# Optimization experiments

Measured on AMD Instinct MI355X. Metric: run time of the kernel, lower is better.

The kernel has to match this reference:

```python
import jax, jax.numpy as jnp
import numpy as np

B, N, D = 2, 2048, 768
H = 12
DH = D // H
SCALE = DH ** -0.5


def setup_inputs() -> dict:
    key = jax.random.key(0)
    k1, k2, k3 = jax.random.split(key, 3)
    x = jax.random.normal(k1, (B, N, D), dtype=jnp.float32)
    w_qkv = jax.random.normal(k2, (D, 3 * D), dtype=jnp.float32) * (D ** -0.5)
    b_qkv = jnp.zeros((3 * D,), dtype=jnp.float32)
    w_proj = jax.random.normal(k3, (D, D), dtype=jnp.float32) * (D ** -0.5)
    b_proj = jnp.zeros((D,), dtype=jnp.float32)
    return {"x": x, "w_qkv": w_qkv, "b_qkv": b_qkv, "w_proj": w_proj, "b_proj": b_proj}


def reference(x, w_qkv, b_qkv, w_proj, b_proj):
    b, n, d = x.shape
    # qkv: (B, n, 3, H, DH) -> (3, B, H, n, DH)
    qkv = (x @ w_qkv + b_qkv).reshape(b, n, 3, H, DH).transpose(2, 0, 3, 1, 4)
    q, k, v = qkv[0], qkv[1], qkv[2]
    # naive full attention matrix (B, H, n, n)
    attn = jnp.einsum('bhqd,bhkd->bhqk', q, k) * SCALE
    attn = jax.nn.softmax(attn, axis=-1)
    out = jnp.einsum('bhqk,bhkd->bhqd', attn, v)  # (B, H, n, DH)
    out = out.transpose(0, 2, 1, 3).reshape(b, n, d)
    return out @ w_proj + b_proj
```

## Files before the change

kernel.cpp:

```cpp
#include <hip/hip_runtime.h>


#define CB 2
#define CN 2048
#define CD 768
#define CH 12
#define CDH 64
#define CEXPSCALE 0.18033688f

typedef __bf16 bf16x8 __attribute__((ext_vector_type(8)));
typedef float f32x4 __attribute__((ext_vector_type(4)));
typedef unsigned short u16x8 __attribute__((ext_vector_type(8)));

static __device__ __forceinline__ unsigned short f2bf(float f) {
  union { float f; unsigned u; } v; v.f = f;
  unsigned r = v.u + 0x7fffu + ((v.u >> 16) & 1u);
  return (unsigned short)(r >> 16);
}

static __device__ __forceinline__ void gld_lds16(const unsigned short* g, unsigned short* lds_base) {
  __builtin_amdgcn_global_load_lds(
      (const __attribute__((address_space(1))) unsigned int*)g,
      (__attribute__((address_space(3))) unsigned int*)(unsigned int)(unsigned long long)lds_base,
      16, 0, 0);
}

__global__ __launch_bounds__(256) void cvt8(const float* __restrict__ src,
                                            unsigned short* __restrict__ dst) {
  size_t i = ((size_t)blockIdx.x * 256 + threadIdx.x) * 8;
  f32x4 a = *(const f32x4*)&src[i];
  f32x4 b = *(const f32x4*)&src[i + 4];
  u16x8 o;
#pragma unroll
  for (int j = 0; j < 4; ++j) { o[j] = f2bf(a[j]); o[4 + j] = f2bf(b[j]); }
  *(u16x8*)&dst[i] = o;
}

__global__ __launch_bounds__(256) void transpose_cvt(const float* __restrict__ src,
                                                     unsigned short* __restrict__ dst,
                                                     int R, int C) {
  __shared__ __align__(16) unsigned short t[64][72];
  const int c0 = blockIdx.x * 64, r0 = blockIdx.y * 64;
  const int tid = threadIdx.x;
#pragma unroll
  for (int i = 0; i < 4; ++i) {
    int c = tid + i * 256;
    int row = c >> 4, cc = (c & 15) * 4;
    f32x4 v = *(const f32x4*)&src[(size_t)(r0 + row) * C + c0 + cc];
#pragma unroll
    for (int j = 0; j < 4; ++j) t[row][cc + j] = f2bf(v[j]);
  }
  __syncthreads();
#pragma unroll
  for (int i = 0; i < 2; ++i) {
    int c = tid + i * 256;
    int drow = c >> 3, rc = (c & 7) * 8;
    u16x8 v;
#pragma unroll
    for (int j = 0; j < 8; ++j) v[j] = t[rc + j][drow];
    *(u16x8*)&dst[(size_t)(c0 + drow) * R + r0 + rc] = v;
  }
}

__global__ __launch_bounds__(256) void gemm128(const unsigned short* __restrict__ A,
                                               const unsigned short* __restrict__ Bt,
                                               const float* __restrict__ bias,
                                               int M, int N, int K, int mode,
                                               unsigned short* __restrict__ o0,
                                               unsigned short* __restrict__ o1,
                                               unsigned short* __restrict__ o2,
                                               float* __restrict__ outF) {
  __shared__ __align__(16) unsigned short As[128 * 32];
  __shared__ __align__(16) unsigned short Bs[128 * 32];
  const int tid = threadIdx.x;
  const int w = tid >> 6, lane = tid & 63, quad = lane >> 4, lc = lane & 15;
  const int wm = (w >> 1) * 64, wn = (w & 1) * 64;
  const int row0 = blockIdx.y * 128, col0 = blockIdx.x * 128;
  f32x4 acc[4][4] = {};

  const int rl = lane >> 2, cl = lane & 3;
  const int gc = cl ^ ((rl >> 1) & 3);
  const int rsw = (lc >> 1) & 3;

  for (int k0 = 0; k0 < K; k0 += 32) {
#pragma unroll
    for (int j = 0; j < 2; ++j) {
      int r = w * 32 + j * 16 + rl;
      gld_lds16(&A[(size_t)(row0 + r) * K + k0 + gc * 8], &As[(w * 32 + j * 16) * 32]);
      gld_lds16(&Bt[(size_t)(col0 + r) * K + k0 + gc * 8], &Bs[(w * 32 + j * 16) * 32]);
    }
    __syncthreads();
    bf16x8 af[4], bfv[4];
#pragma unroll
    for (int mt = 0; mt < 4; ++mt)
      af[mt] = *(const bf16x8*)&As[(wm + mt * 16 + lc) * 32 + (quad ^ rsw) * 8];
#pragma unroll
    for (int nt = 0; nt < 4; ++nt)
      bfv[nt] = *(const bf16x8*)&Bs[(wn + nt * 16 + lc) * 32 + (quad ^ rsw) * 8];
#pragma unroll
    for (int mt = 0; mt < 4; ++mt)
#pragma unroll
      for (int nt = 0; nt < 4; ++nt)
        acc[mt][nt] = __builtin_amdgcn_mfma_f32_16x16x32_bf16(af[mt], bfv[nt], acc[mt][nt], 0, 0, 0);
    __syncthreads();
  }

#pragma unroll
  for (int mt = 0; mt < 4; ++mt) {
#pragma unroll
    for (int nt = 0; nt < 4; ++nt) {
#pragma unroll
      for (int r = 0; r < 4; ++r) {
        int i = row0 + wm + mt * 16 + quad * 4 + r;
        int j = col0 + wn + nt * 16 + lc;
        float v = acc[mt][nt][r] + bias[j];
        if (mode == 0) {
          int b = i >> 11, n = i & 2047;
          int sec = j / 768;
          int within = j - sec * 768;
          int h = within >> 6, d = within & 63;
          int bh = b * CH + h;
          if (sec == 0)      o0[((size_t)bh * CN + n) * CDH + d] = f2bf(v);
          else if (sec == 1) o1[((size_t)bh * CN + n) * CDH + d] = f2bf(v);
          else               o2[((size_t)bh * CDH + d) * CN + n] = f2bf(v);
        } else {
          outF[(size_t)i * N + j] = v;
        }
      }
    }
  }
}

__global__ __launch_bounds__(256, 3) void attn64(const unsigned short* __restrict__ Q,
                                                 const unsigned short* __restrict__ K,
                                                 const unsigned short* __restrict__ Vt,
                                                 unsigned short* __restrict__ O) {
  __shared__ __align__(16) unsigned short Kls[2][64 * 64];
  __shared__ __align__(16) unsigned short Vls[2][64 * 64];
  __shared__ __align__(16) unsigned short P[4][16][88];
  const int bh = blockIdx.x, qt = blockIdx.y;
  const int tid = threadIdx.x;
  const int w = tid >> 6, lane = tid & 63, quad = lane >> 4, lc = lane & 15;
  const unsigned short* Qb = Q + (size_t)bh * CN * CDH;
  const unsigned short* Kb = K + (size_t)bh * CN * CDH;
  const unsigned short* Vb = Vt + (size_t)bh * CDH * CN;
  const int q0 = qt * 64 + w * 16;

  const int sr = lane >> 3, sc = lane & 7;
  const int sg = sc ^ sr;
  const int ksw = lc & 7;
  const int c0r = quad ^ ksw;
  const int c1r = c0r ^ 4;

  bf16x8 qf0 = *(const bf16x8*)&Qb[(size_t)(q0 + lc) * CDH + quad * 8];
  bf16x8 qf1 = *(const bf16x8*)&Qb[(size_t)(q0 + lc) * CDH + 32 + quad * 8];

  f32x4 o[4] = {};
  float rs = 0.f;

#pragma unroll
  for (int j2 = 0; j2 < 2; ++j2) {
    int j = w * 2 + j2;
    int r = j * 8 + sr;
    gld_lds16(&Kb[(size_t)r * CDH + sg * 8], &Kls[0][j * 8 * 64]);
    gld_lds16(&Vb[(size_t)r * CN + 0 + sg * 8], &Vls[0][j * 8 * 64]);
  }

  for (int kt = 0; kt < CN / 64; ++kt) {
    const int bb = kt & 1;
    __syncthreads();
    if (kt + 1 < CN / 64) {
      const int kn = (kt + 1) * 64;
#pragma unroll
      for (int j2 = 0; j2 < 2; ++j2) {
        int j = w * 2 + j2;
        int r = j * 8 + sr;
        gld_lds16(&Kb[(size_t)(kn + r) * CDH + sg * 8], &Kls[bb ^ 1][j * 8 * 64]);
        gld_lds16(&Vb[(size_t)r * CN + kn + sg * 8], &Vls[bb ^ 1][j * 8 * 64]);
      }
    }
#pragma unroll
    for (int t = 0; t < 4; ++t) {
      bf16x8 kf0 = *(const bf16x8*)&Kls[bb][(t * 16 + lc) * 64 + c0r * 8];
      bf16x8 kf1 = *(const bf16x8*)&Kls[bb][(t * 16 + lc) * 64 + c1r * 8];
      f32x4 z = {0.f, 0.f, 0.f, 0.f};
      z = __builtin_amdgcn_mfma_f32_16x16x32_bf16(kf0, qf0, z, 0, 0, 0);
      z = __builtin_amdgcn_mfma_f32_16x16x32_bf16(kf1, qf1, z, 0, 0, 0);
      float p0 = exp2f(z[0] * CEXPSCALE);
      float p1 = exp2f(z[1] * CEXPSCALE);
      float p2 = exp2f(z[2] * CEXPSCALE);
      float p3 = exp2f(z[3] * CEXPSCALE);
      rs += (p0 + p1) + (p2 + p3);
      unsigned d0 = __builtin_amdgcn_perm(__float_as_uint(p1), __float_as_uint(p0), 0x07060302u);
      unsigned d1 = __builtin_amdgcn_perm(__float_as_uint(p3), __float_as_uint(p2), 0x07060302u);
      uint2 dd; dd.x = d0; dd.y = d1;
      *(uint2*)&P[w][lc][t * 16 + quad * 4] = dd;
    }
    asm volatile("s_waitcnt lgkmcnt(0)" ::: "memory");
    bf16x8 pf0 = *(const bf16x8*)&P[w][lc][quad * 8];
    bf16x8 pf1 = *(const bf16x8*)&P[w][lc][32 + quad * 8];
#pragma unroll
    for (int dt = 0; dt < 4; ++dt) {
      bf16x8 vf0 = *(const bf16x8*)&Vls[bb][(dt * 16 + lc) * 64 + c0r * 8];
      bf16x8 vf1 = *(const bf16x8*)&Vls[bb][(dt * 16 + lc) * 64 + c1r * 8];
      o[dt] = __builtin_amdgcn_mfma_f32_16x16x32_bf16(pf0, vf0, o[dt], 0, 0, 0);
      o[dt] = __builtin_amdgcn_mfma_f32_16x16x32_bf16(pf1, vf1, o[dt], 0, 0, 0);
    }
  }

  rs += __shfl_xor(rs, 16, 64);
  rs += __shfl_xor(rs, 32, 64);
  const int b = bh / CH, h = bh - b * CH;
#pragma unroll
  for (int r = 0; r < 4; ++r) {
    float lr = __shfl(rs, quad * 4 + r, 64);
    float inv = 1.0f / lr;
#pragma unroll
    for (int dt = 0; dt < 4; ++dt) {
      int i = b * CN + q0 + quad * 4 + r;
      int j = h * CDH + dt * 16 + lc;
      O[(size_t)i * CD + j] = f2bf(o[dt][r] * inv);
    }
  }
}

extern "C" void kernel_launch(void* const* d_in, const int* in_sizes, int n_in,
                              void* d_out, int out_size, void* d_ws, size_t ws_size,
                              hipStream_t stream) {
  const float* x      = (const float*)d_in[0];
  const float* w_qkv  = (const float*)d_in[1];
  const float* b_qkv  = (const float*)d_in[2];
  const float* w_proj = (const float*)d_in[3];
  const float* b_proj = (const float*)d_in[4];
  float* out = (float*)d_out;
  unsigned short* ws = (unsigned short*)d_ws;

  unsigned short* xb      = ws;
  unsigned short* wqkv_t  = xb + (size_t)4096 * 768;
  unsigned short* wproj_t = wqkv_t + (size_t)2304 * 768;
  unsigned short* Qs  = wproj_t + (size_t)768 * 768;
  unsigned short* Ks  = Qs  + (size_t)CB * CH * CN * CDH;
  unsigned short* Vts = Ks  + (size_t)CB * CH * CN * CDH;
  unsigned short* AO  = Vts + (size_t)CB * CH * CN * CDH;

  cvt8<<<(4096 * 768) / (256 * 8), 256, 0, stream>>>(x, xb);
  transpose_cvt<<<dim3(2304 / 64, 768 / 64), 256, 0, stream>>>(w_qkv, wqkv_t, 768, 2304);
  transpose_cvt<<<dim3(768 / 64, 768 / 64), 256, 0, stream>>>(w_proj, wproj_t, 768, 768);
  gemm128<<<dim3(2304 / 128, 4096 / 128), 256, 0, stream>>>(
      xb, wqkv_t, b_qkv, 4096, 2304, 768, 0, Qs, Ks, Vts, nullptr);
  attn64<<<dim3(CB * CH, CN / 64), 256, 0, stream>>>(Qs, Ks, Vts, AO);
  gemm128<<<dim3(768 / 128, 4096 / 128), 256, 0, stream>>>(
      AO, wproj_t, b_proj, 4096, 768, 768, 1, nullptr, nullptr, nullptr, out);
}
```

Measured before the change: 192.5 us.

## Process two query subtiles per wave in attention and stage V-transpose stores through LDS

Each attention wave now handles 32 query rows as two 16-row subtiles, so every K/V fragment read from LDS feeds twice as many MFMAs and the grid is halved. The softmax scale is folded into Q inside the QKV GEMM epilogue, which removes a multiply per score. The transposed V output of the QKV GEMM is staged through dynamic shared memory so global stores are 16-byte contiguous instead of scattered 2-byte writes. The trade-off is higher register pressure in attention, fewer blocks to spread across CUs, and an extra barrier plus LDS round trip in the GEMM epilogue.

```diff
diff --git a/kernel.cpp b/kernel.cpp
--- a/kernel.cpp
+++ b/kernel.cpp
@@ -62,6 +62,7 @@
   }
 }
 
+extern __shared__ __align__(16) unsigned short smem[];
 __global__ __launch_bounds__(256) void gemm128(const unsigned short* __restrict__ A,
                                                const unsigned short* __restrict__ Bt,
                                                const float* __restrict__ bias,
@@ -70,8 +71,9 @@
                                                unsigned short* __restrict__ o1,
                                                unsigned short* __restrict__ o2,
                                                float* __restrict__ outF) {
-  __shared__ __align__(16) unsigned short As[128 * 32];
-  __shared__ __align__(16) unsigned short Bs[128 * 32];
+  unsigned short* As = smem;
+  unsigned short* Bs = smem + 128 * 32;
+  unsigned short* Ct = smem;
   const int tid = threadIdx.x;
   const int w = tid >> 6, lane = tid & 63, quad = lane >> 4, lc = lane & 15;
   const int wm = (w >> 1) * 64, wn = (w & 1) * 64;
@@ -105,26 +107,57 @@
     __syncthreads();
   }
 
-#pragma unroll
-  for (int mt = 0; mt < 4; ++mt) {
-#pragma unroll
-    for (int nt = 0; nt < 4; ++nt) {
-#pragma unroll
-      for (int r = 0; r < 4; ++r) {
-        int i = row0 + wm + mt * 16 + quad * 4 + r;
-        int j = col0 + wn + nt * 16 + lc;
-        float v = acc[mt][nt][r] + bias[j];
-        if (mode == 0) {
-          int b = i >> 11, n = i & 2047;
-          int sec = j / 768;
-          int within = j - sec * 768;
-          int h = within >> 6, d = within & 63;
-          int bh = b * CH + h;
-          if (sec == 0)      o0[((size_t)bh * CN + n) * CDH + d] = f2bf(v);
-          else if (sec == 1) o1[((size_t)bh * CN + n) * CDH + d] = f2bf(v);
-          else               o2[((size_t)bh * CDH + d) * CN + n] = f2bf(v);
-        } else {
-          outF[(size_t)i * N + j] = v;
+  if (mode == 0 && col0 >= 1536) {
+#pragma unroll
+    for (int mt = 0; mt < 4; ++mt) {
+#pragma unroll
+      for (int nt = 0; nt < 4; ++nt) {
+        int jl = wn + nt * 16 + lc;
+        int il0 = wm + mt * 16 + quad * 4;
+        unsigned short a0 = f2bf(acc[mt][nt][0] + bias[col0 + jl]);
+        unsigned short a1 = f2bf(acc[mt][nt][1] + bias[col0 + jl]);
+        unsigned short a2 = f2bf(acc[mt][nt][2] + bias[col0 + jl]);
+        unsigned short a3 = f2bf(acc[mt][nt][3] + bias[col0 + jl]);
+        uint2 dd;
+        dd.x = (unsigned)a0 | ((unsigned)a1 << 16);
+        dd.y = (unsigned)a2 | ((unsigned)a3 << 16);
+        *(uint2*)&Ct[jl * 136 + il0] = dd;
+      }
+    }
+    __syncthreads();
+    const int b = row0 >> 11, n0 = row0 & 2047;
+#pragma unroll
+    for (int i = 0; i < 8; ++i) {
+      int c = tid + i * 256;
+      int jl = c >> 4, cc = (c & 15) * 8;
+      u16x8 v = *(const u16x8*)&Ct[jl * 136 + cc];
+      int jcol = col0 - 1536 + jl;
+      int h = jcol >> 6, d = jcol & 63;
+      size_t gr = ((size_t)(b * CH + h) * CDH + d);
+      *(u16x8*)&o2[gr * CN + n0 + cc] = v;
+    }
+  } else {
+#pragma unroll
+    for (int mt = 0; mt < 4; ++mt) {
+#pragma unroll
+      for (int nt = 0; nt < 4; ++nt) {
+#pragma unroll
+        for (int r = 0; r < 4; ++r) {
+          int i = row0 + wm + mt * 16 + quad * 4 + r;
+          int j = col0 + wn + nt * 16 + lc;
+          float v = acc[mt][nt][r] + bias[j];
+          if (mode == 0) {
+            int b = i >> 11, n = i & 2047;
+            int sec = j >> 9 >= 3 ? (j >= 1536 ? 2 : 1) : (j >= 768 ? 1 : 0);
+            sec = (j >= 1536) ? 2 : (j >= 768 ? 1 : 0);
+            int within = j - sec * 768;
+            int h = within >> 6, d = within & 63;
+            int bh = b * CH + h;
+            if (sec == 0)      o0[((size_t)bh * CN + n) * CDH + d] = f2bf(v * CEXPSCALE);
+            else               o1[((size_t)bh * CN + n) * CDH + d] = f2bf(v);
+          } else {
+            outF[(size_t)i * N + j] = v;
+          }
         }
       }
     }
@@ -137,14 +170,14 @@
                                                  unsigned short* __restrict__ O) {
   __shared__ __align__(16) unsigned short Kls[2][64 * 64];
   __shared__ __align__(16) unsigned short Vls[2][64 * 64];
-  __shared__ __align__(16) unsigned short P[4][16][88];
+  __shared__ __align__(16) unsigned short P[4][2][16 * 72];
   const int bh = blockIdx.x, qt = blockIdx.y;
   const int tid = threadIdx.x;
   const int w = tid >> 6, lane = tid & 63, quad = lane >> 4, lc = lane & 15;
   const unsigned short* Qb = Q + (size_t)bh * CN * CDH;
   const unsigned short* Kb = K + (size_t)bh * CN * CDH;
   const unsigned short* Vb = Vt + (size_t)bh * CDH * CN;
-  const int q0 = qt * 64 + w * 16;
+  const int q0 = qt * 128 + w * 32;
 
   const int sr = lane >> 3, sc = lane & 7;
   const int sg = sc ^ sr;
@@ -152,11 +185,15 @@
   const int c0r = quad ^ ksw;
   const int c1r = c0r ^ 4;
 
-  bf16x8 qf0 = *(const bf16x8*)&Qb[(size_t)(q0 + lc) * CDH + quad * 8];
-  bf16x8 qf1 = *(const bf16x8*)&Qb[(size_t)(q0 + lc) * CDH + 32 + quad * 8];
-
-  f32x4 o[4] = {};
-  float rs = 0.f;
+  bf16x8 qf[2][2];
+#pragma unroll
+  for (int s = 0; s < 2; ++s) {
+    qf[s][0] = *(const bf16x8*)&Qb[(size_t)(q0 + s * 16 + lc) * CDH + quad * 8];
+    qf[s][1] = *(const bf16x8*)&Qb[(size_t)(q0 + s * 16 + lc) * CDH + 32 + quad * 8];
+  }
+
+  f32x4 o[2][4] = {};
+  float rs[2] = {0.f, 0.f};
 
 #pragma unroll
   for (int j2 = 0; j2 < 2; ++j2) {
@@ -183,43 +220,57 @@
     for (int t = 0; t < 4; ++t) {
       bf16x8 kf0 = *(const bf16x8*)&Kls[bb][(t * 16 + lc) * 64 + c0r * 8];
       bf16x8 kf1 = *(const bf16x8*)&Kls[bb][(t * 16 + lc) * 64 + c1r * 8];
-      f32x4 z = {0.f, 0.f, 0.f, 0.f};
-      z = __builtin_amdgcn_mfma_f32_16x16x32_bf16(kf0, qf0, z, 0, 0, 0);
-      z = __builtin_amdgcn_mfma_f32_16x16x32_bf16(kf1, qf1, z, 0, 0, 0);
-      float p0 = exp2f(z[0] * CEXPSCALE);
-      float p1 = exp2f(z[1] * CEXPSCALE);
-      float p2 = exp2f(z[2] * CEXPSCALE);
-      float p3 = exp2f(z[3] * CEXPSCALE);
-      rs += (p0 + p1) + (p2 + p3);
-      unsigned d0 = __builtin_amdgcn_perm(__float_as_uint(p1), __float_as_uint(p0), 0x07060302u);
-      unsigned d1 = __builtin_amdgcn_perm(__float_as_uint(p3), __float_as_uint(p2), 0x07060302u);
-      uint2 dd; dd.x = d0; dd.y = d1;
-      *(uint2*)&P[w][lc][t * 16 + quad * 4] = dd;
+#pragma unroll
+      for (int s = 0; s < 2; ++s) {
+        f32x4 z = {0.f, 0.f, 0.f, 0.f};
+        z = __builtin_amdgcn_mfma_f32_16x16x32_bf16(kf0, qf[s][0], z, 0, 0, 0);
+        z = __builtin_amdgcn_mfma_f32_16x16x32_bf16(kf1, qf[s][1], z, 0, 0, 0);
+        float p0 = exp2f(z[0]);
+        float p1 = exp2f(z[1]);
+        float p2 = exp2f(z[2]);
+        float p3 = exp2f(z[3]);
+        rs[s] += (p0 + p1) + (p2 + p3);
+        unsigned d0 = __builtin_amdgcn_perm(__float_as_uint(p1), __float_as_uint(p0), 0x07060302u);
+        unsigned d1 = __builtin_amdgcn_perm(__float_as_uint(p3), __float_as_uint(p2), 0x07060302u);
+        uint2 dd; dd.x = d0; dd.y = d1;
+        *(uint2*)&P[w][s][lc * 72 + t * 16 + quad * 4] = dd;
+      }
     }
     asm volatile("s_waitcnt lgkmcnt(0)" ::: "memory");
-    bf16x8 pf0 = *(const bf16x8*)&P[w][lc][quad * 8];
-    bf16x8 pf1 = *(const bf16x8*)&P[w][lc][32 + quad * 8];
+    bf16x8 pf[2][2];
+#pragma unroll
+    for (int s = 0; s < 2; ++s) {
+      pf[s][0] = *(const bf16x8*)&P[w][s][lc * 72 + quad * 8];
+      pf[s][1] = *(const bf16x8*)&P[w][s][lc * 72 + 32 + quad * 8];
+    }
 #pragma unroll
     for (int dt = 0; dt < 4; ++dt) {
       bf16x8 vf0 = *(const bf16x8*)&Vls[bb][(dt * 16 + lc) * 64 + c0r * 8];
       bf16x8 vf1 = *(const bf16x8*)&Vls[bb][(dt * 16 + lc) * 64 + c1r * 8];
-      o[dt] = __builtin_amdgcn_mfma_f32_16x16x32_bf16(pf0, vf0, o[dt], 0, 0, 0);
-      o[dt] = __builtin_amdgcn_mfma_f32_16x16x32_bf16(pf1, vf1, o[dt], 0, 0, 0);
-    }
-  }
-
-  rs += __shfl_xor(rs, 16, 64);
-  rs += __shfl_xor(rs, 32, 64);
+#pragma unroll
+      for (int s = 0; s < 2; ++s) {
+        o[s][dt] = __builtin_amdgcn_mfma_f32_16x16x32_bf16(pf[s][0], vf0, o[s][dt], 0, 0, 0);
+        o[s][dt] = __builtin_amdgcn_mfma_f32_16x16x32_bf16(pf[s][1], vf1, o[s][dt], 0, 0, 0);
+      }
+    }
+  }
+
   const int b = bh / CH, h = bh - b * CH;
 #pragma unroll
-  for (int r = 0; r < 4; ++r) {
-    float lr = __shfl(rs, quad * 4 + r, 64);
-    float inv = 1.0f / lr;
-#pragma unroll
-    for (int dt = 0; dt < 4; ++dt) {
-      int i = b * CN + q0 + quad * 4 + r;
-      int j = h * CDH + dt * 16 + lc;
-      O[(size_t)i * CD + j] = f2bf(o[dt][r] * inv);
+  for (int s = 0; s < 2; ++s) {
+    float r2 = rs[s];
+    r2 += __shfl_xor(r2, 16, 64);
+    r2 += __shfl_xor(r2, 32, 64);
+#pragma unroll
+    for (int r = 0; r < 4; ++r) {
+      float lr = __shfl(r2, quad * 4 + r, 64);
+      float inv = 1.0f / lr;
+#pragma unroll
+      for (int dt = 0; dt < 4; ++dt) {
+        int i = b * CN + q0 + s * 16 + quad * 4 + r;
+        int j = h * CDH + dt * 16 + lc;
+        O[(size_t)i * CD + j] = f2bf(o[s][dt][r] * inv);
+      }
     }
   }
 }
@@ -243,12 +294,15 @@
   unsigned short* Vts = Ks  + (size_t)CB * CH * CN * CDH;
   unsigned short* AO  = Vts + (size_t)CB * CH * CN * CDH;
 
+  const size_t smem_qkv  = (size_t)(128 * 136) * 2;
+  const size_t smem_proj = (size_t)(128 * 32 * 2) * 2;
+
   cvt8<<<(4096 * 768) / (256 * 8), 256, 0, stream>>>(x, xb);
   transpose_cvt<<<dim3(2304 / 64, 768 / 64), 256, 0, stream>>>(w_qkv, wqkv_t, 768, 2304);
   transpose_cvt<<<dim3(768 / 64, 768 / 64), 256, 0, stream>>>(w_proj, wproj_t, 768, 768);
-  gemm128<<<dim3(2304 / 128, 4096 / 128), 256, 0, stream>>>(
+  gemm128<<<dim3(2304 / 128, 4096 / 128), 256, smem_qkv, stream>>>(
       xb, wqkv_t, b_qkv, 4096, 2304, 768, 0, Qs, Ks, Vts, nullptr);
-  attn64<<<dim3(CB * CH, CN / 64), 256, 0, stream>>>(Qs, Ks, Vts, AO);
-  gemm128<<<dim3(768 / 128, 4096 / 128), 256, 0, stream>>>(
+  attn64<<<dim3(CB * CH, CN / 128), 256, 0, stream>>>(Qs, Ks, Vts, AO);
+  gemm128<<<dim3(768 / 128, 4096 / 128), 256, smem_proj, stream>>>(
       AO, wproj_t, b_proj, 4096, 768, 768, 1, nullptr, nullptr, nullptr, out);
 }
```

New measurement: 207.0 us. 1.08x slower.

## Fuse prep kernels, stage V-transpose epilogue through LDS, fold softmax scale into Q

Applied to the files above, without the earlier changes.

The three conversion kernels (x cast, w_qkv and w_proj transpose-casts) are merged into one prep launch to save launch overhead. In the QKV GEMM, the V section's transposed output is first staged in LDS and then written with coalesced 16-byte stores, replacing scattered 2-byte strided writes. The softmax exp scale is folded into Q at the GEMM epilogue, which removes a multiply per score in the attention inner loop. The cost is a larger dynamic shared-memory allocation for the QKV GEMM, which may reduce occupancy, and a slight change in Q rounding.

```diff
diff --git a/kernel.cpp b/kernel.cpp
--- a/kernel.cpp
+++ b/kernel.cpp
@@ -25,23 +25,28 @@
       16, 0, 0);
 }
 
-__global__ __launch_bounds__(256) void cvt8(const float* __restrict__ src,
-                                            unsigned short* __restrict__ dst) {
-  size_t i = ((size_t)blockIdx.x * 256 + threadIdx.x) * 8;
-  f32x4 a = *(const f32x4*)&src[i];
-  f32x4 b = *(const f32x4*)&src[i + 4];
-  u16x8 o;
-#pragma unroll
-  for (int j = 0; j < 4; ++j) { o[j] = f2bf(a[j]); o[4 + j] = f2bf(b[j]); }
-  *(u16x8*)&dst[i] = o;
-}
-
-__global__ __launch_bounds__(256) void transpose_cvt(const float* __restrict__ src,
-                                                     unsigned short* __restrict__ dst,
-                                                     int R, int C) {
+__global__ __launch_bounds__(256) void prep(const float* __restrict__ x,
+                                            unsigned short* __restrict__ xb,
+                                            const float* __restrict__ w_qkv,
+                                            unsigned short* __restrict__ wqkv_t,
+                                            const float* __restrict__ w_proj,
+                                            unsigned short* __restrict__ wproj_t) {
   __shared__ __align__(16) unsigned short t[64][72];
-  const int c0 = blockIdx.x * 64, r0 = blockIdx.y * 64;
-  const int tid = threadIdx.x;
+  const int bid = blockIdx.x, tid = threadIdx.x;
+#pragma unroll
+  for (int it = 0; it < 2; ++it) {
+    size_t i = ((size_t)(bid * 2 + it) * 256 + tid) * 8;
+    f32x4 a = *(const f32x4*)&x[i];
+    f32x4 b = *(const f32x4*)&x[i + 4];
+    u16x8 o;
+#pragma unroll
+    for (int j = 0; j < 4; ++j) { o[j] = f2bf(a[j]); o[4 + j] = f2bf(b[j]); }
+    *(u16x8*)&xb[i] = o;
+  }
+  if (bid >= 576) return;
+  const float* src; unsigned short* dst; int R, C, c0, r0;
+  if (bid < 432) { src = w_qkv; dst = wqkv_t; R = 768; C = 2304; c0 = (bid % 36) * 64; r0 = (bid / 36) * 64; }
+  else { int u = bid - 432; src = w_proj; dst = wproj_t; R = 768; C = 768; c0 = (u % 12) * 64; r0 = (u / 12) * 64; }
 #pragma unroll
   for (int i = 0; i < 4; ++i) {
     int c = tid + i * 256;
@@ -62,6 +67,7 @@
   }
 }
 
+extern __shared__ __align__(16) unsigned short smem[];
 __global__ __launch_bounds__(256) void gemm128(const unsigned short* __restrict__ A,
                                                const unsigned short* __restrict__ Bt,
                                                const float* __restrict__ bias,
@@ -70,8 +76,9 @@
                                                unsigned short* __restrict__ o1,
                                                unsigned short* __restrict__ o2,
                                                float* __restrict__ outF) {
-  __shared__ __align__(16) unsigned short As[128 * 32];
-  __shared__ __align__(16) unsigned short Bs[128 * 32];
+  unsigned short* As = smem;
+  unsigned short* Bs = smem + 128 * 32;
+  unsigned short* Ct = smem;
   const int tid = threadIdx.x;
   const int w = tid >> 6, lane = tid & 63, quad = lane >> 4, lc = lane & 15;
   const int wm = (w >> 1) * 64, wn = (w & 1) * 64;
@@ -105,26 +112,57 @@
     __syncthreads();
   }
 
-#pragma unroll
-  for (int mt = 0; mt < 4; ++mt) {
-#pragma unroll
-    for (int nt = 0; nt < 4; ++nt) {
-#pragma unroll
-      for (int r = 0; r < 4; ++r) {
-        int i = row0 + wm + mt * 16 + quad * 4 + r;
-        int j = col0 + wn + nt * 16 + lc;
-        float v = acc[mt][nt][r] + bias[j];
-        if (mode == 0) {
-          int b = i >> 11, n = i & 2047;
-          int sec = j / 768;
-          int within = j - sec * 768;
-          int h = within >> 6, d = within & 63;
-          int bh = b * CH + h;
-          if (sec == 0)      o0[((size_t)bh * CN + n) * CDH + d] = f2bf(v);
-          else if (sec == 1) o1[((size_t)bh * CN + n) * CDH + d] = f2bf(v);
-          else               o2[((size_t)bh * CDH + d) * CN + n] = f2bf(v);
-        } else {
-          outF[(size_t)i * N + j] = v;
+  if (mode == 0 && col0 >= 1536) {
+#pragma unroll
+    for (int mt = 0; mt < 4; ++mt) {
+#pragma unroll
+      for (int nt = 0; nt < 4; ++nt) {
+        int jl = wn + nt * 16 + lc;
+        int il0 = wm + mt * 16 + quad * 4;
+        float bj = bias[col0 + jl];
+        unsigned short a0 = f2bf(acc[mt][nt][0] + bj);
+        unsigned short a1 = f2bf(acc[mt][nt][1] + bj);
+        unsigned short a2 = f2bf(acc[mt][nt][2] + bj);
+        unsigned short a3 = f2bf(acc[mt][nt][3] + bj);
+        uint2 dd;
+        dd.x = (unsigned)a0 | ((unsigned)a1 << 16);
+        dd.y = (unsigned)a2 | ((unsigned)a3 << 16);
+        *(uint2*)&Ct[jl * 136 + il0] = dd;
+      }
+    }
+    __syncthreads();
+    const int b = row0 >> 11, n0 = row0 & 2047;
+#pragma unroll
+    for (int i = 0; i < 8; ++i) {
+      int c = tid + i * 256;
+      int jl = c >> 4, cc = (c & 15) * 8;
+      u16x8 v = *(const u16x8*)&Ct[jl * 136 + cc];
+      int jcol = col0 - 1536 + jl;
+      int h = jcol >> 6, d = jcol & 63;
+      size_t gr = ((size_t)(b * CH + h) * CDH + d);
+      *(u16x8*)&o2[gr * CN + n0 + cc] = v;
+    }
+  } else {
+#pragma unroll
+    for (int mt = 0; mt < 4; ++mt) {
+#pragma unroll
+      for (int nt = 0; nt < 4; ++nt) {
+#pragma unroll
+        for (int r = 0; r < 4; ++r) {
+          int i = row0 + wm + mt * 16 + quad * 4 + r;
+          int j = col0 + wn + nt * 16 + lc;
+          float v = acc[mt][nt][r] + bias[j];
+          if (mode == 0) {
+            int b = i >> 11, n = i & 2047;
+            int sec = (j >= 768) ? 1 : 0;
+            int within = j - sec * 768;
+            int h = within >> 6, d = within & 63;
+            int bh = b * CH + h;
+            if (sec == 0) o0[((size_t)bh * CN + n) * CDH + d] = f2bf(v * CEXPSCALE);
+            else          o1[((size_t)bh * CN + n) * CDH + d] = f2bf(v);
+          } else {
+            outF[(size_t)i * N + j] = v;
+          }
         }
       }
     }
@@ -186,10 +224,10 @@
       f32x4 z = {0.f, 0.f, 0.f, 0.f};
       z = __builtin_amdgcn_mfma_f32_16x16x32_bf16(kf0, qf0, z, 0, 0, 0);
       z = __builtin_amdgcn_mfma_f32_16x16x32_bf16(kf1, qf1, z, 0, 0, 0);
-      float p0 = exp2f(z[0] * CEXPSCALE);
-      float p1 = exp2f(z[1] * CEXPSCALE);
-      float p2 = exp2f(z[2] * CEXPSCALE);
-      float p3 = exp2f(z[3] * CEXPSCALE);
+      float p0 = exp2f(z[0]);
+      float p1 = exp2f(z[1]);
+      float p2 = exp2f(z[2]);
+      float p3 = exp2f(z[3]);
       rs += (p0 + p1) + (p2 + p3);
       unsigned d0 = __builtin_amdgcn_perm(__float_as_uint(p1), __float_as_uint(p0), 0x07060302u);
       unsigned d1 = __builtin_amdgcn_perm(__float_as_uint(p3), __float_as_uint(p2), 0x07060302u);
@@ -243,12 +281,13 @@
   unsigned short* Vts = Ks  + (size_t)CB * CH * CN * CDH;
   unsigned short* AO  = Vts + (size_t)CB * CH * CN * CDH;
 
-  cvt8<<<(4096 * 768) / (256 * 8), 256, 0, stream>>>(x, xb);
-  transpose_cvt<<<dim3(2304 / 64, 768 / 64), 256, 0, stream>>>(w_qkv, wqkv_t, 768, 2304);
-  transpose_cvt<<<dim3(768 / 64, 768 / 64), 256, 0, stream>>>(w_proj, wproj_t, 768, 768);
-  gemm128<<<dim3(2304 / 128, 4096 / 128), 256, 0, stream>>>(
+  const size_t smem_qkv  = (size_t)(128 * 136) * 2;
+  const size_t smem_proj = (size_t)(128 * 32 * 2) * 2;
+
+  prep<<<768, 256, 0, stream>>>(x, xb, w_qkv, wqkv_t, w_proj, wproj_t);
+  gemm128<<<dim3(2304 / 128, 4096 / 128), 256, smem_qkv, stream>>>(
       xb, wqkv_t, b_qkv, 4096, 2304, 768, 0, Qs, Ks, Vts, nullptr);
   attn64<<<dim3(CB * CH, CN / 64), 256, 0, stream>>>(Qs, Ks, Vts, AO);
-  gemm128<<<dim3(768 / 128, 4096 / 128), 256, 0, stream>>>(
+  gemm128<<<dim3(768 / 128, 4096 / 128), 256, smem_proj, stream>>>(
       AO, wproj_t, b_proj, 4096, 768, 768, 1, nullptr, nullptr, nullptr, out);
 }
```

Measured after the change: 192.2 us. About the same (-0.1%).
